# Performance work log

Hardware: AMD Instinct MI355X
Metric: run time of the kernel (lower is better)

Reference implementation:

```python
import jax, jax.numpy as jnp
import numpy as np

N_NODES = 50000
N_EDGES = 600000
D = 128


def _mean_agg(h, src, dst, n_nodes):
    # DGL SAGEConv 'mean': mean of incoming src features per dst node; 0 for isolated nodes
    s = jax.ops.segment_sum(h[src], dst, num_segments=n_nodes)  # [N, d]
    deg = jax.ops.segment_sum(jnp.ones_like(dst, dtype=h.dtype), dst, num_segments=n_nodes)
    return s / jnp.maximum(deg, 1.0)[:, None]


def setup_inputs() -> dict:
    key = jax.random.key(0)
    ks = jax.random.split(key, 10)
    sc = 1.0 / np.sqrt(D)
    return {
        "x": jax.random.normal(ks[0], (N_NODES, D), jnp.float32),
        "e": jax.random.normal(ks[1], (N_EDGES, D), jnp.float32),
        "src": jax.random.randint(ks[2], (N_EDGES,), 0, N_NODES, jnp.int32),
        "dst": jax.random.randint(ks[3], (N_EDGES,), 0, N_NODES, jnp.int32),
        "W1_self": jax.random.normal(ks[4], (D, D), jnp.float32) * sc,
        "W1_neigh": jax.random.normal(ks[5], (D, D), jnp.float32) * sc,
        "b1": jnp.zeros((D,), jnp.float32),
        "W2_self": jax.random.normal(ks[6], (D, D), jnp.float32) * sc,
        "W2_neigh": jax.random.normal(ks[7], (D, D), jnp.float32) * sc,
        "b2": jnp.zeros((D,), jnp.float32),
        "Wp": jax.random.normal(ks[8], (2 * D, 3), jnp.float32) * (1.0 / np.sqrt(2 * D)),
        "bp": jnp.zeros((3,), jnp.float32),
    }


def reference(x, e, src, dst, W1_self, W1_neigh, b1, W2_self, W2_neigh, b2, Wp, bp):
    n = x.shape[0]
    # SAGEConv 1 (mean) + ReLU
    agg1 = _mean_agg(x, src, dst, n)
    h = jax.nn.relu(x @ W1_self + agg1 @ W1_neigh + b1)
    # SAGEConv 2 (mean)
    agg2 = _mean_agg(h, src, dst, n)
    h = h @ W2_self + agg2 @ W2_neigh + b2
    # MLPPredictor: per-edge gather, concat, linear (edge feature e unused in score)
    he = jnp.concatenate([h[src], h[dst]], axis=1)  # [E, 2D]
    score = he @ Wp + bp  # [E, 3]
    return score
```

## Files before the change

### kernel.cpp

```cpp
#include <hip/hip_runtime.h>
#include <hip/hip_bf16.h>


typedef __attribute__((ext_vector_type(8))) short bf16x8;
typedef __attribute__((ext_vector_type(4))) float f32x4;

static __device__ __forceinline__ float bf16lo(unsigned u) {
    return __uint_as_float(u << 16);
}
static __device__ __forceinline__ float bf16hi(unsigned u) {
    return __uint_as_float(u & 0xffff0000u);
}
static __device__ __forceinline__ unsigned short f2bf(float f) {
    unsigned u = __float_as_uint(f);
    unsigned r = 0x7fffu + ((u >> 16) & 1u);
    return (unsigned short)((u + r) >> 16);
}
static __device__ __forceinline__ unsigned pack_bf162(float a, float b) {
    return (unsigned)f2bf(a) | ((unsigned)f2bf(b) << 16);
}

#define SORT_BLOCKS 128

__global__ __launch_bounds__(256) void k_misc(
    const float* __restrict__ x, unsigned short* __restrict__ xb,
    const int* __restrict__ dst, int* __restrict__ H,
    const float* __restrict__ W1s, const float* __restrict__ W1n,
    unsigned short* __restrict__ Wt1,
    const float* __restrict__ W2s, const float* __restrict__ W2n,
    const float* __restrict__ Wp, const float* __restrict__ b2,
    const float* __restrict__ bp, float* __restrict__ Wc,
    float* __restrict__ bconst, int N, int E, int CHUNK)
{
    const int nCvt = (N * 32 + 255) / 256;
    const int b = blockIdx.x;
    const int t = threadIdx.x;

    if (b < nCvt) {
        int i = b * 256 + t;
        if (i < N * 32) {
            float4 v = ((const float4*)x)[i];
            uint2 o;
            o.x = pack_bf162(v.x, v.y);
            o.y = pack_bf162(v.z, v.w);
            *(uint2*)(xb + (size_t)i * 4) = o;
        }
    } else if (b < nCvt + SORT_BLOCKS) {
        __shared__ int hist[256];
        hist[t] = 0;
        __syncthreads();
        int blk = b - nCvt;
        int start = blk * CHUNK;
        int end = min(start + CHUNK, E);
        for (int e = start + t; e < end; e += 256)
            atomicAdd(&hist[((unsigned)dst[e]) >> 8], 1);
        __syncthreads();
        H[blk * 256 + t] = hist[t];
    } else if (b < nCvt + SORT_BLOCKS + 128) {
        int id = (b - nCvt - SORT_BLOCKS) * 256 + t;
        int k = id >> 7, n = id & 127;
        float v = (k < 128) ? W1s[k * 128 + n] : W1n[(k - 128) * 128 + n];
        Wt1[n * 256 + k] = f2bf(v);
    } else {
        for (int id = t; id < 1539; id += 256) {
            if (id < 1536) {
                int c = id / 12, j = id % 12;
                int q = j / 3, jj = j % 3;
                const float* W2 = (q == 0 || q == 2) ? W2s : W2n;
                int wpoff = (q < 2) ? 0 : 128;
                float s = 0.f;
                for (int m = 0; m < 128; ++m)
                    s += W2[c * 128 + m] * Wp[(wpoff + m) * 3 + jj];
                Wc[c * 12 + j] = s;
            } else {
                int jj = id - 1536;
                float s = bp[jj];
                for (int m = 0; m < 128; ++m)
                    s += b2[m] * (Wp[m * 3 + jj] + Wp[(128 + m) * 3 + jj]);
                bconst[jj] = s;
            }
        }
    }
}

__global__ __launch_bounds__(256) void k_s3(const int* __restrict__ src,
                                            const int* __restrict__ dst,
                                            const int* __restrict__ H,
                                            int* __restrict__ packed,
                                            int* __restrict__ bucketBase,
                                            int E, int CHUNK) {
    __shared__ int lt[256];
    __shared__ int cur[256];
    const int t = threadIdx.x, blk = blockIdx.x;
    int tot = 0, pre = 0;
    for (int b = 0; b < SORT_BLOCKS; ++b) {
        int h = H[b * 256 + t];
        pre += (b < blk) ? h : 0;
        tot += h;
    }
    lt[t] = tot;
    __syncthreads();
    for (int off = 1; off < 256; off <<= 1) {
        int u = (t >= off) ? lt[t - off] : 0;
        __syncthreads();
        lt[t] += u;
        __syncthreads();
    }
    int excl = lt[t] - tot;
    cur[t] = excl + pre;
    if (blk == 0) {
        bucketBase[t] = excl;
        if (t == 0) bucketBase[256] = E;
    }
    __syncthreads();
    int start = blk * CHUNK, end = min(start + CHUNK, E);
    for (int e = start + t; e < end; e += 256) {
        int d = dst[e];
        int p = atomicAdd(&cur[((unsigned)d) >> 8], 1);
        packed[p] = (src[e] & 0xFFFF) | ((d & 255) << 16);
    }
}

__global__ __launch_bounds__(256) void k_s4(const int* __restrict__ packed,
                                            const int* __restrict__ bucketBase,
                                            int* __restrict__ eidx,
                                            int* __restrict__ cursor,
                                            float* __restrict__ fdeg,
                                            float* __restrict__ invdeg, int N) {
    const int t = threadIdx.x, b = blockIdx.x;
    const int rb = bucketBase[b], re = bucketBase[b + 1];
    __shared__ int cnt[256];
    __shared__ int lt[256];
    __shared__ int cur[256];
    cnt[t] = 0;
    __syncthreads();
    for (int i = rb + t; i < re; i += 256)
        atomicAdd(&cnt[(packed[i] >> 16) & 255], 1);
    __syncthreads();
    int v = cnt[t];
    lt[t] = v;
    __syncthreads();
    for (int off = 1; off < 256; off <<= 1) {
        int u = (t >= off) ? lt[t - off] : 0;
        __syncthreads();
        lt[t] += u;
        __syncthreads();
    }
    int excl = lt[t] - v;
    int node = b * 256 + t;
    if (node < N) {
        cursor[node] = rb + excl + v;
        fdeg[node] = (float)v;
        invdeg[node] = 1.0f / fmaxf((float)v, 1.0f);
    }
    cur[t] = rb + excl;
    __syncthreads();
    for (int i = rb + t; i < re; i += 256) {
        int p = packed[i];
        int pos = atomicAdd(&cur[(p >> 16) & 255], 1);
        eidx[pos] = p & 0xFFFF;
    }
}

__global__ __launch_bounds__(256) void k_gemm_fused(
    const unsigned short* __restrict__ xb,
    const int* __restrict__ eidx, const int* __restrict__ cursor,
    const float* __restrict__ fdeg, const float* __restrict__ invdeg,
    const unsigned short* __restrict__ Wt, const float* __restrict__ bias,
    const float* __restrict__ Wc, float* __restrict__ P, int N)
{
    __shared__ __align__(16) char sW[65536];
    __shared__ float sWc[1536];
    const int t = threadIdx.x;
    const int wave = t >> 6, lane = t & 63;
    const int nodeBase = blockIdx.x * 128 + wave * 32;
    const int lrow = lane & 15, lk = lane >> 4;
    const int r0 = nodeBase + lrow, r1 = nodeBase + 16 + lrow;

    int* eidxL = (int*)sW;
    const int nb0 = blockIdx.x * 128;
    const int lastN = min(nb0 + 127, N - 1);
    const int estart = cursor[nb0] - (int)fdeg[nb0];
    const int eend = cursor[lastN];
    const int ecnt = eend - estart;
    const bool ldsOK = (ecnt <= 16384);
    if (ldsOK) {
        for (int i = t; i < ecnt; i += 256) eidxL[i] = eidx[estart + i];
    }
    __syncthreads();

    int d0 = 0, d1 = 0;
    if (r0 < N) d0 = (int)fdeg[r0];
    if (r1 < N) d1 = (int)fdeg[r1];
    const int* EP;
    int o0, o1;
    if (ldsOK) {
        EP = eidxL;
        o0 = (r0 < N) ? cursor[r0] - d0 - estart : 0;
        o1 = (r1 < N) ? cursor[r1] - d1 - estart : 0;
    } else {
        EP = eidx;
        o0 = (r0 < N) ? cursor[r0] - d0 : 0;
        o1 = (r1 < N) ? cursor[r1] - d1 : 0;
    }

    float agg0[4][8], agg1[4][8];
#pragma unroll
    for (int k = 0; k < 4; ++k)
#pragma unroll
        for (int i = 0; i < 8; ++i) { agg0[k][i] = 0.f; agg1[k][i] = 0.f; }

#define ACC32(AGG, V)                                                   \
    _Pragma("unroll") for (int k = 0; k < 4; ++k) {                     \
        AGG[k][0] += bf16lo(V[k].x); AGG[k][1] += bf16hi(V[k].x);       \
        AGG[k][2] += bf16lo(V[k].y); AGG[k][3] += bf16hi(V[k].y);       \
        AGG[k][4] += bf16lo(V[k].z); AGG[k][5] += bf16hi(V[k].z);       \
        AGG[k][6] += bf16lo(V[k].w); AGG[k][7] += bf16hi(V[k].w);       \
    }

    const int dmax = max(d0, d1);
    for (int j = 0; j < dmax; j += 2) {
        int sA = (j < d0) ? EP[o0 + j] : -1;
        int sB = (j + 1 < d0) ? EP[o0 + j + 1] : -1;
        int sC = (j < d1) ? EP[o1 + j] : -1;
        int sD = (j + 1 < d1) ? EP[o1 + j + 1] : -1;
        const unsigned short* rA = xb + (size_t)max(sA, 0) * 128 + lk * 8;
        const unsigned short* rB = xb + (size_t)max(sB, 0) * 128 + lk * 8;
        const unsigned short* rC = xb + (size_t)max(sC, 0) * 128 + lk * 8;
        const unsigned short* rD = xb + (size_t)max(sD, 0) * 128 + lk * 8;
        uint4 vA[4], vB[4], vC[4], vD[4];
#pragma unroll
        for (int k = 0; k < 4; ++k) {
            vA[k] = *(const uint4*)(rA + k * 32);
            vB[k] = *(const uint4*)(rB + k * 32);
            vC[k] = *(const uint4*)(rC + k * 32);
            vD[k] = *(const uint4*)(rD + k * 32);
        }
        if (sA >= 0) ACC32(agg0, vA)
        if (sB >= 0) ACC32(agg0, vB)
        if (sC >= 0) ACC32(agg1, vC)
        if (sD >= 0) ACC32(agg1, vD)
    }
#undef ACC32

    union { bf16x8 v; unsigned u[4]; } afrag0[4], afrag1[4];
    {
        float sc0 = (r0 < N) ? invdeg[r0] : 0.f;
        float sc1 = (r1 < N) ? invdeg[r1] : 0.f;
#pragma unroll
        for (int k = 0; k < 4; ++k)
#pragma unroll
            for (int i = 0; i < 4; ++i) {
                afrag0[k].u[i] = pack_bf162(agg0[k][2 * i] * sc0,
                                            agg0[k][2 * i + 1] * sc0);
                afrag1[k].u[i] = pack_bf162(agg1[k][2 * i] * sc1,
                                            agg1[k][2 * i + 1] * sc1);
            }
    }

    __syncthreads();
#pragma unroll
    for (int i = 0; i < 16; ++i) {
        int o = (i * 256 + t) * 16;
        int n = o >> 9;
        int c = o & 511;
        int sw = (n << 9) | (c ^ ((n & 7) << 4));
        *(float4*)&sW[sw] = *(const float4*)((const char*)Wt + o);
    }
    for (int i = t; i < 1536; i += 256) sWc[i] = Wc[i];

    f32x4 acc[2][8];
#pragma unroll
    for (int rs = 0; rs < 2; ++rs)
#pragma unroll
        for (int nb = 0; nb < 8; ++nb) acc[rs][nb] = (f32x4){0.f, 0.f, 0.f, 0.f};

    __syncthreads();

    for (int ks = 0; ks < 8; ++ks) {
        bf16x8 a0, a1;
        if (ks < 4) {
            const int kk = ks * 32 + lk * 8;
            a0 = (bf16x8){};
            a1 = (bf16x8){};
            if (r0 < N) a0 = *(const bf16x8*)(xb + (size_t)r0 * 128 + kk);
            if (r1 < N) a1 = *(const bf16x8*)(xb + (size_t)r1 * 128 + kk);
        } else {
            a0 = afrag0[ks - 4].v;
            a1 = afrag1[ks - 4].v;
        }
        const int cbase = ks * 64 + lk * 16;
#pragma unroll
        for (int nb = 0; nb < 8; ++nb) {
            int n = nb * 16 + lrow;
            int sw = (n << 9) | (cbase ^ ((n & 7) << 4));
            bf16x8 b = *(const bf16x8*)&sW[sw];
            acc[0][nb] = __builtin_amdgcn_mfma_f32_16x16x32_bf16(a0, b, acc[0][nb], 0, 0, 0);
            acc[1][nb] = __builtin_amdgcn_mfma_f32_16x16x32_bf16(a1, b, acc[1][nb], 0, 0, 0);
        }
    }

#pragma unroll
    for (int rs = 0; rs < 2; ++rs) {
        float hval[8][4];
#pragma unroll
        for (int nb = 0; nb < 8; ++nb) {
            float bv = bias[nb * 16 + lrow];
#pragma unroll
            for (int r = 0; r < 4; ++r)
                hval[nb][r] = fmaxf(acc[rs][nb][r] + bv, 0.f);
        }
#pragma unroll
        for (int r = 0; r < 4; ++r) {
            float pj[12];
#pragma unroll
            for (int j = 0; j < 12; ++j) pj[j] = 0.f;
#pragma unroll
            for (int nb = 0; nb < 8; ++nb) {
                float hv = hval[nb][r];
                const float* wrow = &sWc[(nb * 16 + lrow) * 12];
#pragma unroll
                for (int j = 0; j < 12; ++j) pj[j] += hv * wrow[j];
            }
#pragma unroll
            for (int off = 8; off; off >>= 1) {
#pragma unroll
                for (int j = 0; j < 12; ++j) pj[j] += __shfl_xor(pj[j], off, 64);
            }
            int node = nodeBase + rs * 16 + lk * 4 + r;
            if (lrow == 0 && node < N) {
                float* prow = &P[(size_t)node * 16];
                *(float4*)(prow + 0)  = make_float4(pj[0], pj[1], pj[2], pj[6]);
                *(float4*)(prow + 4)  = make_float4(pj[7], pj[8], 0.f, 0.f);
                *(float4*)(prow + 8)  = make_float4(pj[3], pj[4], pj[5], pj[9]);
                *(float4*)(prow + 12) = make_float4(pj[10], pj[11], 0.f, 0.f);
            }
        }
    }
}

__global__ __launch_bounds__(256) void k_agg3(const float* __restrict__ P,
                                              const int* __restrict__ eidx,
                                              const int* __restrict__ cursor,
                                              const float* __restrict__ fdeg,
                                              const float* __restrict__ invdeg,
                                              float4* __restrict__ ps4,
                                              float4* __restrict__ pd4, int N) {
    int g = blockIdx.x * 256 + threadIdx.x;
    if (g >= N) return;
    int d = (int)fdeg[g];
    int o = cursor[g] - d;
    float a0 = 0.f, a1 = 0.f, a2 = 0.f, a3 = 0.f, a4 = 0.f, a5 = 0.f;
    int i = 0;
    for (; i + 2 <= d; i += 2) {
        int s0 = eidx[o + i], s1 = eidx[o + i + 1];
        float4 u0 = *(const float4*)&P[(size_t)s0 * 16 + 8];
        float4 u1 = *(const float4*)&P[(size_t)s0 * 16 + 12];
        float4 w0 = *(const float4*)&P[(size_t)s1 * 16 + 8];
        float4 w1 = *(const float4*)&P[(size_t)s1 * 16 + 12];
        a0 += u0.x; a1 += u0.y; a2 += u0.z; a3 += u0.w; a4 += u1.x; a5 += u1.y;
        a0 += w0.x; a1 += w0.y; a2 += w0.z; a3 += w0.w; a4 += w1.x; a5 += w1.y;
    }
    if (i < d) {
        int s0 = eidx[o + i];
        float4 u0 = *(const float4*)&P[(size_t)s0 * 16 + 8];
        float4 u1 = *(const float4*)&P[(size_t)s0 * 16 + 12];
        a0 += u0.x; a1 += u0.y; a2 += u0.z; a3 += u0.w; a4 += u1.x; a5 += u1.y;
    }
    float sc = invdeg[g];
    float4 s0v = *(const float4*)&P[(size_t)g * 16];
    float4 s1v = *(const float4*)&P[(size_t)g * 16 + 4];
    ps4[g] = make_float4(s0v.x + a0 * sc, s0v.y + a1 * sc, s0v.z + a2 * sc, 0.f);
    pd4[g] = make_float4(s0v.w + a3 * sc, s1v.x + a4 * sc, s1v.y + a5 * sc, 0.f);
}

__global__ void k_edge(const float4* __restrict__ ps4, const float4* __restrict__ pd4,
                       const int* __restrict__ src, const int* __restrict__ dst,
                       const float* __restrict__ bconst, float* __restrict__ out, int E)
{
    int e = blockIdx.x * blockDim.x + threadIdx.x;
    if (e >= E) return;
    float4 a = ps4[src[e]];
    float4 b = pd4[dst[e]];
    out[(size_t)e * 3 + 0] = a.x + b.x + bconst[0];
    out[(size_t)e * 3 + 1] = a.y + b.y + bconst[1];
    out[(size_t)e * 3 + 2] = a.z + b.z + bconst[2];
}

extern "C" void kernel_launch(void* const* d_in, const int* in_sizes, int n_in,
                              void* d_out, int out_size, void* d_ws, size_t ws_size,
                              hipStream_t stream)
{
    const float* x   = (const float*)d_in[0];
    const int*   src = (const int*)d_in[2];
    const int*   dst = (const int*)d_in[3];
    const float* W1s = (const float*)d_in[4];
    const float* W1n = (const float*)d_in[5];
    const float* b1  = (const float*)d_in[6];
    const float* W2s = (const float*)d_in[7];
    const float* W2n = (const float*)d_in[8];
    const float* b2  = (const float*)d_in[9];
    const float* Wp  = (const float*)d_in[10];
    const float* bp  = (const float*)d_in[11];
    const int N = in_sizes[0] / 128;
    const int E = in_sizes[2];
    float* out = (float*)d_out;

    const int NB = (N + 255) / 256;
    const int CHUNK = (E + SORT_BLOCKS - 1) / SORT_BLOCKS;

    char* wsp = (char*)d_ws;
    auto alloc = [&](size_t bytes) { char* p = wsp; wsp += (bytes + 255) & ~(size_t)255; return p; };
    float* fdeg     = (float*)alloc((size_t)N * 4);
    float* invdeg   = (float*)alloc((size_t)N * 4);
    int*   cursor   = (int*)alloc((size_t)N * 4);
    int*   eidx     = (int*)alloc((size_t)E * 4);
    int*   packed   = (int*)alloc((size_t)E * 4);
    int*   H        = (int*)alloc((size_t)SORT_BLOCKS * 256 * 4);
    int*   bucketBase = (int*)alloc(260 * 4);
    unsigned short* xb  = (unsigned short*)alloc((size_t)N * 128 * 2);
    unsigned short* Wt1 = (unsigned short*)alloc(256 * 128 * 2);
    float* Wc     = (float*)alloc(1536 * 4);
    float* bconst = (float*)alloc(256);
    float* P      = (float*)alloc((size_t)N * 16 * 4);
    float* ps4    = (float*)alloc((size_t)N * 16);
    float* pd4    = (float*)alloc((size_t)N * 16);

    const int nCvt = (N * 32 + 255) / 256;
    k_misc<<<nCvt + SORT_BLOCKS + 129, 256, 0, stream>>>(
        x, xb, dst, H, W1s, W1n, Wt1, W2s, W2n, Wp, b2, bp, Wc, bconst, N, E, CHUNK);

    k_s3<<<SORT_BLOCKS, 256, 0, stream>>>(src, dst, H, packed, bucketBase, E, CHUNK);
    k_s4<<<NB, 256, 0, stream>>>(packed, bucketBase, eidx, cursor, fdeg, invdeg, N);

    k_gemm_fused<<<(N + 127) / 128, 256, 0, stream>>>(xb, eidx, cursor, fdeg, invdeg,
                                                      Wt1, b1, Wc, P, N);

    k_agg3<<<(N + 255) / 256, 256, 0, stream>>>(P, eidx, cursor, fdeg, invdeg,
                                                (float4*)ps4, (float4*)pd4, N);

    k_edge<<<(E + 255) / 256, 256, 0, stream>>>((const float4*)ps4, (const float4*)pd4,
                                                src, dst, bconst, out, E);
}
```

Before: 177.3 us.

## Gather neighbor features as fp8 and halve rows per block in fused GEMM

```diff
diff --git a/kernel.cpp b/kernel.cpp
--- a/kernel.cpp
+++ b/kernel.cpp
@@ -4,6 +4,16 @@
 
 typedef __attribute__((ext_vector_type(8))) short bf16x8;
 typedef __attribute__((ext_vector_type(4))) float f32x4;
+typedef __attribute__((ext_vector_type(2))) float f32x2;
+
+#if defined(__has_builtin)
+#if __has_builtin(__builtin_amdgcn_cvt_pk_f32_fp8)
+#define USE_FP8_GATHER 1
+#endif
+#endif
+#ifndef USE_FP8_GATHER
+#define USE_FP8_GATHER 0
+#endif
 
 static __device__ __forceinline__ float bf16lo(unsigned u) {
     return __uint_as_float(u << 16);
@@ -20,10 +30,26 @@
     return (unsigned)f2bf(a) | ((unsigned)f2bf(b) << 16);
 }
 
+static __device__ __forceinline__ unsigned f2fp8(float f) {
+    unsigned b = __float_as_uint(f);
+    unsigned s = (b >> 24) & 0x80u;
+    float af = fabsf(f);
+    unsigned code;
+    if (af < 0.015625f) {
+        code = (unsigned)rintf(af * 512.f);
+    } else {
+        unsigned u = (b & 0x7FFFFFFFu) + 0x7FFFFu + ((b >> 20) & 1u);
+        unsigned e = (u >> 23) - 120u;
+        code = (e << 3) | ((u >> 20) & 7u);
+    }
+    return s | code;
+}
+
 #define SORT_BLOCKS 128
 
 __global__ __launch_bounds__(256) void k_misc(
     const float* __restrict__ x, unsigned short* __restrict__ xb,
+    unsigned char* __restrict__ xq,
     const int* __restrict__ dst, int* __restrict__ H,
     const float* __restrict__ W1s, const float* __restrict__ W1n,
     unsigned short* __restrict__ Wt1,
@@ -44,6 +70,9 @@
             o.x = pack_bf162(v.x, v.y);
             o.y = pack_bf162(v.z, v.w);
             *(uint2*)(xb + (size_t)i * 4) = o;
+            unsigned q = f2fp8(v.x) | (f2fp8(v.y) << 8) |
+                         (f2fp8(v.z) << 16) | (f2fp8(v.w) << 24);
+            *(unsigned*)(xq + (size_t)i * 4) = q;
         }
     } else if (b < nCvt + SORT_BLOCKS) {
         __shared__ int hist[256];
@@ -59,7 +88,19 @@
     } else if (b < nCvt + SORT_BLOCKS + 128) {
         int id = (b - nCvt - SORT_BLOCKS) * 256 + t;
         int k = id >> 7, n = id & 127;
-        float v = (k < 128) ? W1s[k * 128 + n] : W1n[(k - 128) * 128 + n];
+        float v;
+        if (k < 128) {
+            v = W1s[k * 128 + n];
+        } else {
+#if USE_FP8_GATHER
+            int K = k - 128;
+            int ksb = K >> 5, r = K & 31, lkp = r >> 3, i = r & 7;
+            int orig = lkp * 32 + ksb * 8 + i;
+            v = W1n[orig * 128 + n];
+#else
+            v = W1n[(k - 128) * 128 + n];
+#endif
+        }
         Wt1[n * 256 + k] = f2bf(v);
     } else {
         for (int id = t; id < 1539; id += 256) {
@@ -164,6 +205,7 @@
 
 __global__ __launch_bounds__(256) void k_gemm_fused(
     const unsigned short* __restrict__ xb,
+    const unsigned char* __restrict__ xq,
     const int* __restrict__ eidx, const int* __restrict__ cursor,
     const float* __restrict__ fdeg, const float* __restrict__ invdeg,
     const unsigned short* __restrict__ Wt, const float* __restrict__ bias,
@@ -173,13 +215,12 @@
     __shared__ float sWc[1536];
     const int t = threadIdx.x;
     const int wave = t >> 6, lane = t & 63;
-    const int nodeBase = blockIdx.x * 128 + wave * 32;
     const int lrow = lane & 15, lk = lane >> 4;
-    const int r0 = nodeBase + lrow, r1 = nodeBase + 16 + lrow;
+    const int r0 = blockIdx.x * 64 + wave * 16 + lrow;
 
     int* eidxL = (int*)sW;
-    const int nb0 = blockIdx.x * 128;
-    const int lastN = min(nb0 + 127, N - 1);
+    const int nb0 = blockIdx.x * 64;
+    const int lastN = min(nb0 + 63, N - 1);
     const int estart = cursor[nb0] - (int)fdeg[nb0];
     const int eend = cursor[lastN];
     const int ecnt = eend - estart;
@@ -189,73 +230,129 @@
     }
     __syncthreads();
 
-    int d0 = 0, d1 = 0;
-    if (r0 < N) d0 = (int)fdeg[r0];
-    if (r1 < N) d1 = (int)fdeg[r1];
-    const int* EP;
-    int o0, o1;
-    if (ldsOK) {
-        EP = eidxL;
-        o0 = (r0 < N) ? cursor[r0] - d0 - estart : 0;
-        o1 = (r1 < N) ? cursor[r1] - d1 - estart : 0;
-    } else {
-        EP = eidx;
-        o0 = (r0 < N) ? cursor[r0] - d0 : 0;
-        o1 = (r1 < N) ? cursor[r1] - d1 : 0;
-    }
-
-    float agg0[4][8], agg1[4][8];
-#pragma unroll
-    for (int k = 0; k < 4; ++k)
-#pragma unroll
-        for (int i = 0; i < 8; ++i) { agg0[k][i] = 0.f; agg1[k][i] = 0.f; }
-
-#define ACC32(AGG, V)                                                   \
-    _Pragma("unroll") for (int k = 0; k < 4; ++k) {                     \
-        AGG[k][0] += bf16lo(V[k].x); AGG[k][1] += bf16hi(V[k].x);       \
-        AGG[k][2] += bf16lo(V[k].y); AGG[k][3] += bf16hi(V[k].y);       \
-        AGG[k][4] += bf16lo(V[k].z); AGG[k][5] += bf16hi(V[k].z);       \
-        AGG[k][6] += bf16lo(V[k].w); AGG[k][7] += bf16hi(V[k].w);       \
-    }
-
-    const int dmax = max(d0, d1);
-    for (int j = 0; j < dmax; j += 2) {
-        int sA = (j < d0) ? EP[o0 + j] : -1;
-        int sB = (j + 1 < d0) ? EP[o0 + j + 1] : -1;
-        int sC = (j < d1) ? EP[o1 + j] : -1;
-        int sD = (j + 1 < d1) ? EP[o1 + j + 1] : -1;
-        const unsigned short* rA = xb + (size_t)max(sA, 0) * 128 + lk * 8;
-        const unsigned short* rB = xb + (size_t)max(sB, 0) * 128 + lk * 8;
-        const unsigned short* rC = xb + (size_t)max(sC, 0) * 128 + lk * 8;
-        const unsigned short* rD = xb + (size_t)max(sD, 0) * 128 + lk * 8;
-        uint4 vA[4], vB[4], vC[4], vD[4];
-#pragma unroll
-        for (int k = 0; k < 4; ++k) {
-            vA[k] = *(const uint4*)(rA + k * 32);
-            vB[k] = *(const uint4*)(rB + k * 32);
-            vC[k] = *(const uint4*)(rC + k * 32);
-            vD[k] = *(const uint4*)(rD + k * 32);
-        }
-        if (sA >= 0) ACC32(agg0, vA)
-        if (sB >= 0) ACC32(agg0, vB)
-        if (sC >= 0) ACC32(agg1, vC)
-        if (sD >= 0) ACC32(agg1, vD)
-    }
-#undef ACC32
-
-    union { bf16x8 v; unsigned u[4]; } afrag0[4], afrag1[4];
+    union { bf16x8 v; unsigned u[4]; } afrag0[4];
+
+#if USE_FP8_GATHER
+#define ACCQ(AGG, A, B)                                                      \
+    {                                                                        \
+        f32x2 p;                                                             \
+        p = __builtin_amdgcn_cvt_pk_f32_fp8((int)(A).x, false);              \
+        AGG[0][0] += p.x; AGG[0][1] += p.y;                                  \
+        p = __builtin_amdgcn_cvt_pk_f32_fp8((int)(A).x, true);               \
+        AGG[0][2] += p.x; AGG[0][3] += p.y;                                  \
+        p = __builtin_amdgcn_cvt_pk_f32_fp8((int)(A).y, false);              \
+        AGG[0][4] += p.x; AGG[0][5] += p.y;                                  \
+        p = __builtin_amdgcn_cvt_pk_f32_fp8((int)(A).y, true);               \
+        AGG[0][6] += p.x; AGG[0][7] += p.y;                                  \
+        p = __builtin_amdgcn_cvt_pk_f32_fp8((int)(A).z, false);              \
+        AGG[1][0] += p.x; AGG[1][1] += p.y;                                  \
+        p = __builtin_amdgcn_cvt_pk_f32_fp8((int)(A).z, true);               \
+        AGG[1][2] += p.x; AGG[1][3] += p.y;                                  \
+        p = __builtin_amdgcn_cvt_pk_f32_fp8((int)(A).w, false);              \
+        AGG[1][4] += p.x; AGG[1][5] += p.y;                                  \
+        p = __builtin_amdgcn_cvt_pk_f32_fp8((int)(A).w, true);               \
+        AGG[1][6] += p.x; AGG[1][7] += p.y;                                  \
+        p = __builtin_amdgcn_cvt_pk_f32_fp8((int)(B).x, false);              \
+        AGG[2][0] += p.x; AGG[2][1] += p.y;                                  \
+        p = __builtin_amdgcn_cvt_pk_f32_fp8((int)(B).x, true);               \
+        AGG[2][2] += p.x; AGG[2][3] += p.y;                                  \
+        p = __builtin_amdgcn_cvt_pk_f32_fp8((int)(B).y, false);              \
+        AGG[2][4] += p.x; AGG[2][5] += p.y;                                  \
+        p = __builtin_amdgcn_cvt_pk_f32_fp8((int)(B).y, true);               \
+        AGG[2][6] += p.x; AGG[2][7] += p.y;                                  \
+        p = __builtin_amdgcn_cvt_pk_f32_fp8((int)(B).z, false);              \
+        AGG[3][0] += p.x; AGG[3][1] += p.y;                                  \
+        p = __builtin_amdgcn_cvt_pk_f32_fp8((int)(B).z, true);               \
+        AGG[3][2] += p.x; AGG[3][3] += p.y;                                  \
+        p = __builtin_amdgcn_cvt_pk_f32_fp8((int)(B).w, false);              \
+        AGG[3][4] += p.x; AGG[3][5] += p.y;                                  \
+        p = __builtin_amdgcn_cvt_pk_f32_fp8((int)(B).w, true);               \
+        AGG[3][6] += p.x; AGG[3][7] += p.y;                                  \
+    }
+#endif
+
     {
-        float sc0 = (r0 < N) ? invdeg[r0] : 0.f;
-        float sc1 = (r1 < N) ? invdeg[r1] : 0.f;
+        float agg[4][8];
 #pragma unroll
         for (int k = 0; k < 4; ++k)
 #pragma unroll
-            for (int i = 0; i < 4; ++i) {
-                afrag0[k].u[i] = pack_bf162(agg0[k][2 * i] * sc0,
-                                            agg0[k][2 * i + 1] * sc0);
-                afrag1[k].u[i] = pack_bf162(agg1[k][2 * i] * sc1,
-                                            agg1[k][2 * i + 1] * sc1);
-            }
+            for (int i = 0; i < 8; ++i) agg[k][i] = 0.f;
+
+        if (r0 < N) {
+            int d = (int)fdeg[r0];
+            int o;
+            const int* EP;
+            if (ldsOK) { EP = eidxL; o = cursor[r0] - d - estart; }
+            else       { EP = eidx;  o = cursor[r0] - d; }
+            int j = 0;
+#if USE_FP8_GATHER
+            for (; j + 2 <= d; j += 2) {
+                int s0 = EP[o + j], s1 = EP[o + j + 1];
+                const unsigned char* row0 = xq + (size_t)s0 * 128 + lk * 32;
+                const unsigned char* row1 = xq + (size_t)s1 * 128 + lk * 32;
+                uint4 A0 = *(const uint4*)(row0);
+                uint4 B0 = *(const uint4*)(row0 + 16);
+                uint4 A1 = *(const uint4*)(row1);
+                uint4 B1 = *(const uint4*)(row1 + 16);
+                ACCQ(agg, A0, B0)
+                ACCQ(agg, A1, B1)
+            }
+            if (j < d) {
+                int s0 = EP[o + j];
+                const unsigned char* row0 = xq + (size_t)s0 * 128 + lk * 32;
+                uint4 A0 = *(const uint4*)(row0);
+                uint4 B0 = *(const uint4*)(row0 + 16);
+                ACCQ(agg, A0, B0)
+            }
+#else
+            for (; j + 2 <= d; j += 2) {
+                int s0 = EP[o + j], s1 = EP[o + j + 1];
+                const unsigned short* row0 = xb + (size_t)s0 * 128 + lk * 8;
+                const unsigned short* row1 = xb + (size_t)s1 * 128 + lk * 8;
+                uint4 v0[4], v1[4];
+#pragma unroll
+                for (int k = 0; k < 4; ++k) {
+                    v0[k] = *(const uint4*)(row0 + k * 32);
+                    v1[k] = *(const uint4*)(row1 + k * 32);
+                }
+#pragma unroll
+                for (int k = 0; k < 4; ++k) {
+                    agg[k][0] += bf16lo(v0[k].x); agg[k][1] += bf16hi(v0[k].x);
+                    agg[k][2] += bf16lo(v0[k].y); agg[k][3] += bf16hi(v0[k].y);
+                    agg[k][4] += bf16lo(v0[k].z); agg[k][5] += bf16hi(v0[k].z);
+                    agg[k][6] += bf16lo(v0[k].w); agg[k][7] += bf16hi(v0[k].w);
+                    agg[k][0] += bf16lo(v1[k].x); agg[k][1] += bf16hi(v1[k].x);
+                    agg[k][2] += bf16lo(v1[k].y); agg[k][3] += bf16hi(v1[k].y);
+                    agg[k][4] += bf16lo(v1[k].z); agg[k][5] += bf16hi(v1[k].z);
+                    agg[k][6] += bf16lo(v1[k].w); agg[k][7] += bf16hi(v1[k].w);
+                }
+            }
+            if (j < d) {
+                int s0 = EP[o + j];
+                const unsigned short* row0 = xb + (size_t)s0 * 128 + lk * 8;
+#pragma unroll
+                for (int k = 0; k < 4; ++k) {
+                    uint4 v0 = *(const uint4*)(row0 + k * 32);
+                    agg[k][0] += bf16lo(v0.x); agg[k][1] += bf16hi(v0.x);
+                    agg[k][2] += bf16lo(v0.y); agg[k][3] += bf16hi(v0.y);
+                    agg[k][4] += bf16lo(v0.z); agg[k][5] += bf16hi(v0.z);
+                    agg[k][6] += bf16lo(v0.w); agg[k][7] += bf16hi(v0.w);
+                }
+            }
+#endif
+            float sc = invdeg[r0];
+#pragma unroll
+            for (int k = 0; k < 4; ++k)
+#pragma unroll
+                for (int i = 0; i < 4; ++i)
+                    afrag0[k].u[i] = pack_bf162(agg[k][2 * i] * sc,
+                                                agg[k][2 * i + 1] * sc);
+        } else {
+#pragma unroll
+            for (int k = 0; k < 4; ++k)
+#pragma unroll
+                for (int i = 0; i < 4; ++i) afrag0[k].u[i] = 0u;
+        }
     }
 
     __syncthreads();
@@ -269,25 +366,20 @@
     }
     for (int i = t; i < 1536; i += 256) sWc[i] = Wc[i];
 
-    f32x4 acc[2][8];
-#pragma unroll
-    for (int rs = 0; rs < 2; ++rs)
-#pragma unroll
-        for (int nb = 0; nb < 8; ++nb) acc[rs][nb] = (f32x4){0.f, 0.f, 0.f, 0.f};
+    f32x4 acc[8];
+#pragma unroll
+    for (int nb = 0; nb < 8; ++nb) acc[nb] = (f32x4){0.f, 0.f, 0.f, 0.f};
 
     __syncthreads();
 
     for (int ks = 0; ks < 8; ++ks) {
-        bf16x8 a0, a1;
+        bf16x8 a0;
         if (ks < 4) {
             const int kk = ks * 32 + lk * 8;
             a0 = (bf16x8){};
-            a1 = (bf16x8){};
             if (r0 < N) a0 = *(const bf16x8*)(xb + (size_t)r0 * 128 + kk);
-            if (r1 < N) a1 = *(const bf16x8*)(xb + (size_t)r1 * 128 + kk);
         } else {
             a0 = afrag0[ks - 4].v;
-            a1 = afrag1[ks - 4].v;
         }
         const int cbase = ks * 64 + lk * 16;
 #pragma unroll
@@ -295,20 +387,18 @@
             int n = nb * 16 + lrow;
             int sw = (n << 9) | (cbase ^ ((n & 7) << 4));
             bf16x8 b = *(const bf16x8*)&sW[sw];
-            acc[0][nb] = __builtin_amdgcn_mfma_f32_16x16x32_bf16(a0, b, acc[0][nb], 0, 0, 0);
-            acc[1][nb] = __builtin_amdgcn_mfma_f32_16x16x32_bf16(a1, b, acc[1][nb], 0, 0, 0);
-        }
-    }
-
-#pragma unroll
-    for (int rs = 0; rs < 2; ++rs) {
+            acc[nb] = __builtin_amdgcn_mfma_f32_16x16x32_bf16(a0, b, acc[nb], 0, 0, 0);
+        }
+    }
+
+    {
         float hval[8][4];
 #pragma unroll
         for (int nb = 0; nb < 8; ++nb) {
             float bv = bias[nb * 16 + lrow];
 #pragma unroll
             for (int r = 0; r < 4; ++r)
-                hval[nb][r] = fmaxf(acc[rs][nb][r] + bv, 0.f);
+                hval[nb][r] = fmaxf(acc[nb][r] + bv, 0.f);
         }
 #pragma unroll
         for (int r = 0; r < 4; ++r) {
@@ -327,7 +417,7 @@
 #pragma unroll
                 for (int j = 0; j < 12; ++j) pj[j] += __shfl_xor(pj[j], off, 64);
             }
-            int node = nodeBase + rs * 16 + lk * 4 + r;
+            int node = blockIdx.x * 64 + wave * 16 + lk * 4 + r;
             if (lrow == 0 && node < N) {
                 float* prow = &P[(size_t)node * 16];
                 *(float4*)(prow + 0)  = make_float4(pj[0], pj[1], pj[2], pj[6]);
@@ -419,6 +509,7 @@
     int*   H        = (int*)alloc((size_t)SORT_BLOCKS * 256 * 4);
     int*   bucketBase = (int*)alloc(260 * 4);
     unsigned short* xb  = (unsigned short*)alloc((size_t)N * 128 * 2);
+    unsigned char*  xq  = (unsigned char*)alloc((size_t)N * 128);
     unsigned short* Wt1 = (unsigned short*)alloc(256 * 128 * 2);
     float* Wc     = (float*)alloc(1536 * 4);
     float* bconst = (float*)alloc(256);
@@ -428,13 +519,15 @@
 
     const int nCvt = (N * 32 + 255) / 256;
     k_misc<<<nCvt + SORT_BLOCKS + 129, 256, 0, stream>>>(
-        x, xb, dst, H, W1s, W1n, Wt1, W2s, W2n, Wp, b2, bp, Wc, bconst, N, E, CHUNK);
+        x, xb, xq, dst, H, W1s, W1n, Wt1, W2s, W2n, Wp, b2, bp, Wc, bconst,
+        N, E, CHUNK);
 
     k_s3<<<SORT_BLOCKS, 256, 0, stream>>>(src, dst, H, packed, bucketBase, E, CHUNK);
     k_s4<<<NB, 256, 0, stream>>>(packed, bucketBase, eidx, cursor, fdeg, invdeg, N);
 
-    k_gemm_fused<<<(N + 127) / 128, 256, 0, stream>>>(xb, eidx, cursor, fdeg, invdeg,
-                                                      Wt1, b1, Wc, P, N);
+    k_gemm_fused<<<(N + 63) / 64, 256, 0, stream>>>(xb, xq, eidx, cursor,
+                                                    fdeg, invdeg,
+                                                    Wt1, b1, Wc, P, N);
 
     k_agg3<<<(N + 255) / 256, 256, 0, stream>>>(P, eidx, cursor, fdeg, invdeg,
                                                 (float4*)ps4, (float4*)pd4, N);
```

After: 155.3 us, median of 2. 1.14x faster.
